# Performance work log

Measured on AMD Instinct MI355X. Metric: run time of the kernel, lower is better.

Reference implementation:

```python
import jax, jax.numpy as jnp
import numpy as np

DIM = 512
NUM_HEADS = 8
HEAD_DIM = DIM // NUM_HEADS
LOCAL_HEADS = 4
WINDOW = 64
NEG_INF = -1e9


def setup_inputs() -> dict:
    key = jax.random.key(0)
    ks = jax.random.split(key, 5)
    B, N, C = 4, 8192, DIM
    x = jax.random.normal(ks[0], (B, N, C), dtype=jnp.float32)
    # nn.Linear weights stored as [out, in]; xavier-ish scale
    s = (2.0 / (C + C)) ** 0.5
    Wq = jax.random.normal(ks[1], (C, C), dtype=jnp.float32) * s
    Wkv = jax.random.normal(ks[2], (C, C), dtype=jnp.float32) * s
    Wproj = jax.random.normal(ks[3], (C, C), dtype=jnp.float32) * s
    bproj = jax.random.normal(ks[4], (C,), dtype=jnp.float32) * 0.01
    return {"x": x, "Wq": Wq, "Wkv": Wkv, "Wproj": Wproj, "bproj": bproj}


def _look_around(t):
    # t: [B,H,nw,m,d] -> [B,H,nw,3m,d] (prev window, current, next; zero-padded at ends)
    p = jnp.pad(t, ((0, 0), (0, 0), (1, 1), (0, 0), (0, 0)))
    return jnp.concatenate([p[:, :, :-2], p[:, :, 1:-1], p[:, :, 2:]], axis=3)


def _local_attn(q, k, v, m):
    # non-causal LocalAttention, look_backward=1, look_forward=1
    B, H, N, d = q.shape
    nw = N // m
    scale = d ** -0.5
    qw = q.reshape(B, H, nw, m, d)
    kw = _look_around(k.reshape(B, H, nw, m, d))
    vw = _look_around(v.reshape(B, H, nw, m, d))
    # mask out look-around positions that fall outside the sequence
    pos = jnp.arange(N).reshape(nw, m)
    pp = jnp.pad(pos, ((1, 1), (0, 0)), constant_values=-1)
    kpos = jnp.concatenate([pp[:-2], pp[1:-1], pp[2:]], axis=1)  # [nw, 3m]
    valid = (kpos >= 0)[None, None, :, None, :]
    scores = jnp.einsum('bhwid,bhwjd->bhwij', qw * scale, kw)
    scores = jnp.where(valid, scores, NEG_INF)
    attn = jax.nn.softmax(scores, axis=-1)
    out = jnp.einsum('bhwij,bhwjd->bhwid', attn, vw)
    return out.reshape(B, H, N, d)


def _linear_attn(q, k, v):
    d = q.shape[-1]
    q = jax.nn.softmax(q, axis=-1) * (d ** -0.5)
    k = jax.nn.softmax(k, axis=-2)
    context = jnp.einsum('bhnd,bhne->bhde', k, v)
    return jnp.einsum('bhnd,bhde->bhne', q, context)


def reference(x, Wq, Wkv, Wproj, bproj):
    B, N, C = x.shape
    m = WINDOW
    original_N = N
    rem = N % m  # static; 0 for chosen shapes
    if rem > 0:
        x = jnp.pad(x, ((0, 0), (m - rem, 0), (0, 0)))
        N = x.shape[1]
    q = x @ Wq.T
    k = x @ Wkv.T
    v = x @ Wkv.T  # source uses the same kv linear for both k and v
    merge = lambda t: t.reshape(B, N, -1, HEAD_DIM).transpose(0, 2, 1, 3)  # [B,H,N,d]
    q, k, v = merge(q), merge(k), merge(v)
    lh = LOCAL_HEADS
    lq, gq = q[:, :lh], q[:, lh:]
    lk, gk = k[:, :lh], k[:, lh:]
    lv, gv = v[:, :lh], v[:, lh:]
    outs = []
    if lh > 0:
        outs.append(_local_attn(lq, lk, lv, m))
    if q.shape[1] - lh > 0:
        outs.append(_linear_attn(gq, gk, gv))
    attn = jnp.concatenate(outs, axis=1)  # [B,H,N,d]
    y = attn.transpose(0, 2, 1, 3).reshape(B, N, -1)
    y = y[:, -original_N:]
    y = y @ Wproj.T + bproj
    return (y, attn)
```

## Files before the change

### kernel.cpp

```cpp
#include <hip/hip_runtime.h>

#define DIM 512
#define NH 8
#define HD 64
#define LH 4
#define WIN 64
#define BATCH 4
#define SEQ 8192
#define NWIN (SEQ/WIN)

typedef unsigned short u16;
typedef __bf16 bf16x8 __attribute__((ext_vector_type(8)));
typedef float f32x4 __attribute__((ext_vector_type(4)));

__device__ __forceinline__ float b2f(u16 u) {
    return __uint_as_float(((unsigned int)u) << 16);
}
__device__ __forceinline__ u16 f2b(float f) {
    unsigned int x = __float_as_uint(f);
    return (u16)((x + 0x7FFFu + ((x >> 16) & 1u)) >> 16);
}

__device__ __forceinline__ void gload16(const void* g, void* l) {
    __builtin_amdgcn_global_load_lds(
        (__attribute__((address_space(1))) void*)g,
        (__attribute__((address_space(3))) void*)l, 16, 0, 0);
}

__global__ void convert_bf16(const float* __restrict__ src, u16* __restrict__ dst, long n)
{
    long i = ((long)blockIdx.x * 256 + threadIdx.x) * 8;
    const long stride = (long)gridDim.x * 256 * 8;
    for (; i < n; i += stride) {
        uint4 a = *(const uint4*)(src + i), b = *(const uint4*)(src + i + 4);
        const float* af = (const float*)&a;
        const float* bf_ = (const float*)&b;
        uint4 o; u16* ou = (u16*)&o;
        #pragma unroll
        for (int j = 0; j < 4; j++) { ou[j] = f2b(af[j]); ou[4 + j] = f2b(bf_[j]); }
        *(uint4*)(dst + i) = o;
    }
}

__global__ void convert_w3(const float* __restrict__ Wq, const float* __restrict__ Wkv,
                           const float* __restrict__ Wp, u16* __restrict__ Wqk,
                           u16* __restrict__ Wproj_b)
{
    const int slice = blockIdx.y;
    const float* src = (slice == 0) ? Wq : (slice == 1) ? Wkv : Wp;
    u16* dst = (slice == 0) ? Wqk : (slice == 1) ? (Wqk + DIM * DIM) : Wproj_b;
    long i = ((long)blockIdx.x * 256 + threadIdx.x) * 8;
    if (i >= (long)DIM * DIM) return;
    uint4 a = *(const uint4*)(src + i), b = *(const uint4*)(src + i + 4);
    const float* af = (const float*)&a;
    const float* bf_ = (const float*)&b;
    uint4 o; u16* ou = (u16*)&o;
    #pragma unroll
    for (int j = 0; j < 4; j++) { ou[j] = f2b(af[j]); ou[4 + j] = f2b(bf_[j]); }
    *(uint4*)(dst + i) = o;
}

__global__ __launch_bounds__(256) void gemm_qk_tiled(const u16* __restrict__ xb,
        const u16* __restrict__ Wqk, u16* __restrict__ qh, u16* __restrict__ kh)
{
    __shared__ __align__(16) u16 smem[16384];
    u16* lA = smem;
    u16* lB = smem + 4096;

    const int tid = threadIdx.x;
    const int wv = tid >> 6, lane = tid & 63;
    const int quad = lane >> 4, l16 = lane & 15;
    const int wr = wv >> 1, wc = wv & 1;
    const int row0 = blockIdx.y * 128;
    const int col0 = blockIdx.x * 128;
    const int lrow = lane >> 2, lkc = (lane & 3) * 8;

    f32x4 acc[4][4];
    #pragma unroll
    for (int t = 0; t < 4; t++)
        for (int u = 0; u < 4; u++)
            for (int i = 0; i < 4; i++) acc[t][u][i] = 0.f;

    const u16* gA = xb  + (size_t)(row0 + lrow) * DIM + lkc;
    const u16* gB = Wqk + (size_t)(col0 + lrow) * DIM + lkc;

    for (int kt = 0; kt < DIM; kt += 32) {
        __syncthreads();
        #pragma unroll
        for (int i = 0; i < 2; i++) {
            int rb = wv * 32 + i * 16;
            gload16(gA + (size_t)rb * DIM + kt, &lA[rb * 32]);
            gload16(gB + (size_t)rb * DIM + kt, &lB[rb * 32]);
        }
        __syncthreads();
        bf16x8 af[4], bfr[4];
        #pragma unroll
        for (int t = 0; t < 4; t++)
            af[t] = *(const bf16x8*)&lA[(wr * 64 + t * 16 + l16) * 32 + quad * 8];
        #pragma unroll
        for (int u = 0; u < 4; u++)
            bfr[u] = *(const bf16x8*)&lB[(wc * 64 + u * 16 + l16) * 32 + quad * 8];
        #pragma unroll
        for (int t = 0; t < 4; t++)
            #pragma unroll
            for (int u = 0; u < 4; u++)
                acc[t][u] = __builtin_amdgcn_mfma_f32_16x16x32_bf16(af[t], bfr[u], acc[t][u], 0, 0, 0);
    }

    __syncthreads();
    u16* cw = smem + wv * 4096;
    #pragma unroll
    for (int t = 0; t < 4; t++)
        #pragma unroll
        for (int u = 0; u < 4; u++)
            #pragma unroll
            for (int r = 0; r < 4; r++)
                cw[(t * 16 + quad * 4 + r) * 64 + u * 16 + l16] = f2b(acc[t][u][r]);

    const int colg0 = col0 + wc * 64;
    const int seg = lane & 7;
    u16* dstbase;
    {
        int h = (colg0 & 511) >> 6;
        u16* base = (colg0 < 512) ? qh : kh;
        dstbase = base + (size_t)h * SEQ * HD;
    }
    #pragma unroll
    for (int i = 0; i < 8; i++) {
        int mm = i * 8 + (lane >> 3);
        uint4 v = *(const uint4*)&cw[mm * 64 + seg * 8];
        int m = row0 + wr * 64 + mm;
        int bb = m >> 13, nn = m & (SEQ - 1);
        *(uint4*)(dstbase + ((size_t)bb * NH * SEQ + nn) * HD + seg * 8) = v;
    }
}

#define KJ_STRIDE 72
#define KT_STRIDE 200
#define OT_STRIDE 80

__global__ __launch_bounds__(256) void local_attn(const u16* __restrict__ qh,
        const u16* __restrict__ kh, float* __restrict__ attn_out,
        u16* __restrict__ attn_b)
{
    __shared__ __align__(16) u16 kjP[192 * KJ_STRIDE];
    __shared__ __align__(16) u16 kT[64 * KT_STRIDE];

    const int w = blockIdx.x;
    const int bh = blockIdx.y;
    const int b = bh >> 2, h = bh & 3;
    const int tid = threadIdx.x;
    const int wv = tid >> 6, lane = tid & 63;
    const int quad = lane >> 4, l16 = lane & 15;

    for (int idx = tid; idx < 192 * 8; idx += 256) {
        int j = idx >> 3, dc = (idx & 7) << 3;
        int n = w * WIN - WIN + j;
        uint4 val = make_uint4(0, 0, 0, 0);
        if (n >= 0 && n < SEQ)
            val = *(const uint4*)(kh + (((size_t)(b * NH + h)) * SEQ + n) * HD + dc);
        *(uint4*)(&kjP[j * KJ_STRIDE + dc]) = val;
    }
    __syncthreads();
    for (int idx = tid; idx < 64 * 192; idx += 256) {
        int e = idx & 63, j = idx >> 6;
        kT[e * KT_STRIDE + j] = kjP[j * KJ_STRIDE + e];
    }
    __syncthreads();

    f32x4 s[12];
    #pragma unroll
    for (int t = 0; t < 12; t++)
        for (int i = 0; i < 4; i++) s[t][i] = 0.f;

    const u16* qrow = qh + (((size_t)(b * NH + h)) * SEQ + w * WIN + wv * 16 + l16) * HD + quad * 8;
    #pragma unroll
    for (int kk = 0; kk < 64; kk += 32) {
        bf16x8 a = *(const bf16x8*)(qrow + kk);
        #pragma unroll
        for (int t = 0; t < 12; t++) {
            bf16x8 bf = *(const bf16x8*)(&kjP[(t * 16 + l16) * KJ_STRIDE + kk + quad * 8]);
            s[t] = __builtin_amdgcn_mfma_f32_16x16x32_bf16(a, bf, s[t], 0, 0, 0);
        }
    }
    __syncthreads();

    const float scale = 0.125f;
    #pragma unroll
    for (int r = 0; r < 4; r++) {
        float vals[12];
        float mx = -3.0e38f;
        #pragma unroll
        for (int t = 0; t < 12; t++) {
            int j = t * 16 + l16;
            float v = s[t][r] * scale;
            bool valid = !((w == 0 && j < 64) || (w == NWIN - 1 && j >= 128));
            v = valid ? v : -30000.0f;
            vals[t] = v;
            mx = fmaxf(mx, v);
        }
        for (int m = 1; m <= 8; m <<= 1) mx = fmaxf(mx, __shfl_xor(mx, m));
        float sum = 0.f;
        #pragma unroll
        for (int t = 0; t < 12; t++) { vals[t] = __expf(vals[t] - mx); sum += vals[t]; }
        for (int m = 1; m <= 8; m <<= 1) sum += __shfl_xor(sum, m);
        float inv = 1.0f / sum;
        int prow = wv * 16 + quad * 4 + r;
        #pragma unroll
        for (int t = 0; t < 12; t++)
            kjP[prow * KT_STRIDE + t * 16 + l16] = f2b(vals[t] * inv);
    }
    __syncthreads();

    f32x4 o[4];
    #pragma unroll
    for (int t = 0; t < 4; t++)
        for (int i = 0; i < 4; i++) o[t][i] = 0.f;
    #pragma unroll
    for (int kc = 0; kc < 6; kc++) {
        bf16x8 a = *(const bf16x8*)(&kjP[(wv * 16 + l16) * KT_STRIDE + kc * 32 + quad * 8]);
        #pragma unroll
        for (int t = 0; t < 4; t++) {
            bf16x8 bf = *(const bf16x8*)(&kT[(t * 16 + l16) * KT_STRIDE + kc * 32 + quad * 8]);
            o[t] = __builtin_amdgcn_mfma_f32_16x16x32_bf16(a, bf, o[t], 0, 0, 0);
        }
    }
    #pragma unroll
    for (int t = 0; t < 4; t++) {
        int e = t * 16 + l16;
        #pragma unroll
        for (int r = 0; r < 4; r++) {
            int n = w * WIN + wv * 16 + quad * 4 + r;
            attn_out[(((size_t)(b * NH + h)) * SEQ + n) * HD + e] = o[t][r];
        }
    }
    __syncthreads();
    #pragma unroll
    for (int t = 0; t < 4; t++)
        #pragma unroll
        for (int r = 0; r < 4; r++)
            kT[(wv * 16 + quad * 4 + r) * OT_STRIDE + t * 16 + l16] = f2b(o[t][r]);
    __syncthreads();
    for (int idx = tid; idx < 512; idx += 256) {
        int row = idx >> 3, seg = (idx & 7) * 8;
        uint4 v = *(const uint4*)&kT[row * OT_STRIDE + seg];
        *(uint4*)(attn_b + ((size_t)(b * SEQ + w * WIN + row)) * DIM + h * HD + seg) = v;
    }
}

__global__ __launch_bounds__(256) void ctx_accum(const u16* __restrict__ kh,
        float* __restrict__ partials, float* __restrict__ colsum)
{
    const int chunk = blockIdx.x;
    const int bh = blockIdx.y;
    const int b = bh >> 2, hg = bh & 3;
    const int tid = threadIdx.x;
    const int wv = tid >> 6, lane = tid & 63;
    const int d0 = (lane >> 2) * 4;
    const int e0 = (lane & 3) * 16;

    __shared__ __align__(16) float smem[2 * 64 * 68];
    float* kraw = smem;
    float* kexp = smem + 64 * 68;

    f32x4 acc[4][4];
    #pragma unroll
    for (int dd = 0; dd < 4; dd++)
        #pragma unroll
        for (int j = 0; j < 4; j++)
            for (int i = 0; i < 4; i++) acc[dd][j][i] = 0.f;
    f32x4 csum;
    for (int i = 0; i < 4; i++) csum[i] = 0.f;

    const u16* kbase = kh + ((size_t)(b * NH + LH + hg)) * SEQ * HD
                          + (size_t)chunk * 256 * HD;

    for (int ph = 0; ph < 4; ph++) {
        __syncthreads();
        #pragma unroll
        for (int pass = 0; pass < 2; pass++) {
            int idx = pass * 256 + tid;
            int row = idx >> 3, seg = (idx & 7) * 8;
            uint4 v = *(const uint4*)(kbase + ((size_t)(ph * 64 + row)) * HD + seg);
            const u16* u = (const u16*)&v;
            f32x4 r0, r1, E0, E1;
            #pragma unroll
            for (int j = 0; j < 4; j++) {
                r0[j] = b2f(u[j]);      E0[j] = __expf(r0[j]);
                r1[j] = b2f(u[4 + j]);  E1[j] = __expf(r1[j]);
            }
            float* kr = &kraw[row * 68 + seg];
            float* ke = &kexp[row * 68 + seg];
            *(f32x4*)kr = r0;  *(f32x4*)(kr + 4) = r1;
            *(f32x4*)ke = E0;  *(f32x4*)(ke + 4) = E1;
        }
        __syncthreads();
        #pragma unroll 4
        for (int i = 0; i < 16; i++) {
            int roff = (wv * 16 + i) * 68;
            f32x4 ek = *(const f32x4*)&kexp[roff + d0];
            const f32x4* kv = (const f32x4*)&kraw[roff + e0];
            f32x4 k0 = kv[0], k1 = kv[1], k2 = kv[2], k3 = kv[3];
            csum += ek;
            #pragma unroll
            for (int dd = 0; dd < 4; dd++) {
                acc[dd][0] += ek[dd] * k0;
                acc[dd][1] += ek[dd] * k1;
                acc[dd][2] += ek[dd] * k2;
                acc[dd][3] += ek[dd] * k3;
            }
        }
    }

    float* red0 = smem;
    float* red1 = smem + 4160;
    __syncthreads();
    if (wv >= 2) {
        float* rd = (wv == 2) ? red0 : red1;
        #pragma unroll
        for (int dd = 0; dd < 4; dd++)
            #pragma unroll
            for (int j = 0; j < 4; j++)
                *(f32x4*)&rd[(d0 + dd) * 64 + e0 + j * 4] = acc[dd][j];
        if ((lane & 3) == 0) *(f32x4*)&rd[4096 + d0] = csum;
    }
    __syncthreads();
    if (wv < 2) {
        float* rd = (wv == 0) ? red0 : red1;
        #pragma unroll
        for (int dd = 0; dd < 4; dd++)
            #pragma unroll
            for (int j = 0; j < 4; j++)
                acc[dd][j] += *(const f32x4*)&rd[(d0 + dd) * 64 + e0 + j * 4];
        csum += *(const f32x4*)&rd[4096 + d0];
    }
    __syncthreads();
    if (wv == 1) {
        #pragma unroll
        for (int dd = 0; dd < 4; dd++)
            #pragma unroll
            for (int j = 0; j < 4; j++)
                *(f32x4*)&red0[(d0 + dd) * 64 + e0 + j * 4] = acc[dd][j];
        if ((lane & 3) == 0) *(f32x4*)&red0[4096 + d0] = csum;
    }
    __syncthreads();
    if (wv == 0) {
        float* P = partials + ((size_t)(chunk * 16 + bh)) * 4096;
        #pragma unroll
        for (int dd = 0; dd < 4; dd++)
            #pragma unroll
            for (int j = 0; j < 4; j++) {
                f32x4 r = acc[dd][j] + *(const f32x4*)&red0[(d0 + dd) * 64 + e0 + j * 4];
                *(f32x4*)&P[(d0 + dd) * 64 + e0 + j * 4] = r;
            }
        if ((lane & 3) == 0) {
            f32x4 cs = csum + *(const f32x4*)&red0[4096 + d0];
            #pragma unroll
            for (int dd = 0; dd < 4; dd++)
                atomicAdd(colsum + bh * 64 + d0 + dd, cs[dd]);
        }
    }
}

__global__ __launch_bounds__(256) void reduce_ctx(const float* __restrict__ partials,
        const float* __restrict__ colsum, float* __restrict__ ctx)
{
    const int quarter = blockIdx.x;
    const int bh = blockIdx.y;
    const int tid = threadIdx.x;
    __shared__ float cs[64];
    if (tid < 64) cs[tid] = colsum[bh * 64 + tid];
    __syncthreads();
    const int i0 = quarter * 1024;
    for (int idx = i0 + tid; idx < i0 + 1024; idx += 256) {
        float s = 0.f;
        #pragma unroll 8
        for (int c = 0; c < 32; c++)
            s += partials[((size_t)(c * 16 + bh)) * 4096 + idx];
        ctx[(size_t)bh * 4096 + idx] = s / cs[idx >> 6];
    }
}

__global__ __launch_bounds__(256) void global_out(const u16* __restrict__ qh,
        const float* __restrict__ ctxg, float* __restrict__ attn_out,
        u16* __restrict__ attn_b)
{
    const int nblk = blockIdx.x;
    const int bh = blockIdx.y;
    const int b = bh >> 2, hg = bh & 3;
    const int tid = threadIdx.x;

    __shared__ float ctx[4096];
    for (int idx = tid; idx < 4096; idx += 256)
        ctx[idx] = ctxg[(size_t)bh * 4096 + idx];
    __syncthreads();

    const int n = nblk * 256 + tid;
    const size_t rowidx = (((size_t)(b * NH + LH + hg)) * SEQ + n) * HD;
    const u16* qrow = qh + rowidx;

    float sumexp = 0.f;
    for (int c = 0; c < 8; c++) {
        uint4 v = *(const uint4*)(qrow + c * 8);
        const u16* u = (const u16*)&v;
        #pragma unroll
        for (int jj = 0; jj < 8; jj++) sumexp += __expf(b2f(u[jj]));
    }
    float inv = 0.125f / sumexp;

    f32x4 out4[16];
    #pragma unroll
    for (int t = 0; t < 16; t++)
        for (int i = 0; i < 4; i++) out4[t][i] = 0.f;

    for (int c = 0; c < 8; c++) {
        uint4 v = *(const uint4*)(qrow + c * 8);
        const u16* u = (const u16*)&v;
        #pragma unroll
        for (int jj = 0; jj < 8; jj++) {
            float pd = __expf(b2f(u[jj])) * inv;
            const f32x4* cr = (const f32x4*)&ctx[(c * 8 + jj) * 64];
            #pragma unroll
            for (int t = 0; t < 16; t++)
                out4[t] += pd * cr[t];
        }
    }

    float* ao = attn_out + rowidx;
    #pragma unroll
    for (int t = 0; t < 16; t++)
        *(f32x4*)(ao + t * 4) = out4[t];

    u16* ab = attn_b + ((size_t)(b * SEQ + n)) * DIM + (LH + hg) * HD;
    #pragma unroll
    for (int t = 0; t < 8; t++) {
        uint4 o; u16* ou = (u16*)&o;
        #pragma unroll
        for (int j = 0; j < 8; j++) ou[j] = f2b(out4[t * 2 + (j >> 2)][j & 3]);
        *(uint4*)(ab + t * 8) = o;
    }
}

__global__ __launch_bounds__(256) void proj_gemm_tiled(const u16* __restrict__ attn_b,
        const u16* __restrict__ Wproj, const float* __restrict__ bproj,
        float* __restrict__ y)
{
    __shared__ __align__(16) u16 smem[8192];
    u16* lA = smem;
    u16* lB = smem + 4096;

    const int tid = threadIdx.x;
    const int wv = tid >> 6, lane = tid & 63;
    const int quad = lane >> 4, l16 = lane & 15;
    const int wr = wv >> 1, wc = wv & 1;
    const int row0 = blockIdx.y * 128;
    const int col0 = blockIdx.x * 128;
    const int lrow = lane >> 2, lkc = (lane & 3) * 8;

    f32x4 acc[4][4];
    #pragma unroll
    for (int t = 0; t < 4; t++)
        for (int u = 0; u < 4; u++)
            for (int i = 0; i < 4; i++) acc[t][u][i] = 0.f;

    const u16* gA = attn_b + (size_t)(row0 + lrow) * DIM + lkc;
    const u16* gB = Wproj  + (size_t)(col0 + lrow) * DIM + lkc;

    for (int kt = 0; kt < DIM; kt += 32) {
        __syncthreads();
        #pragma unroll
        for (int i = 0; i < 2; i++) {
            int rb = wv * 32 + i * 16;
            gload16(gA + (size_t)rb * DIM + kt, &lA[rb * 32]);
            gload16(gB + (size_t)rb * DIM + kt, &lB[rb * 32]);
        }
        __syncthreads();
        bf16x8 af[4], bfr[4];
        #pragma unroll
        for (int t = 0; t < 4; t++)
            af[t] = *(const bf16x8*)&lA[(wr * 64 + t * 16 + l16) * 32 + quad * 8];
        #pragma unroll
        for (int u = 0; u < 4; u++)
            bfr[u] = *(const bf16x8*)&lB[(wc * 64 + u * 16 + l16) * 32 + quad * 8];
        #pragma unroll
        for (int t = 0; t < 4; t++)
            #pragma unroll
            for (int u = 0; u < 4; u++)
                acc[t][u] = __builtin_amdgcn_mfma_f32_16x16x32_bf16(af[t], bfr[u], acc[t][u], 0, 0, 0);
    }

    #pragma unroll
    for (int u = 0; u < 4; u++) {
        int col = col0 + wc * 64 + u * 16 + l16;
        float bias = bproj[col];
        #pragma unroll
        for (int t = 0; t < 4; t++)
            #pragma unroll
            for (int r = 0; r < 4; r++) {
                int m = row0 + wr * 64 + t * 16 + quad * 4 + r;
                y[(size_t)m * DIM + col] = acc[t][u][r] + bias;
            }
    }
}

extern "C" void kernel_launch(void* const* d_in, const int* in_sizes, int n_in,
                              void* d_out, int out_size, void* d_ws, size_t ws_size,
                              hipStream_t stream)
{
    (void)in_sizes; (void)n_in; (void)out_size; (void)ws_size;
    const float* x     = (const float*)d_in[0];
    const float* Wq    = (const float*)d_in[1];
    const float* Wkv   = (const float*)d_in[2];
    const float* Wproj = (const float*)d_in[3];
    const float* bproj = (const float*)d_in[4];

    float* y        = (float*)d_out;
    float* attn_out = y + (size_t)BATCH * SEQ * DIM;

    u16* xb = (u16*)y;
    u16* qh = xb + (size_t)BATCH * SEQ * DIM;

    float* partials = attn_out + (size_t)LH * SEQ * HD;

    char* ws = (char*)d_ws;
    float* S       = (float*)ws;
    float* colsum  = (float*)(ws + 262144);
    u16*   Wqk     = (u16*)(ws + 266240);
    u16*   Wproj_b = (u16*)(ws + 266240 + 1048576);
    u16*   kh      = (u16*)(ws + 266240 + 1048576 + 524288);
    u16*   attn_b  = kh + (size_t)BATCH * SEQ * DIM;

    const long NX = (long)BATCH * SEQ * DIM;

    hipMemsetAsync(colsum, 0, 4096, stream);
    convert_bf16<<<4096, 256, 0, stream>>>(x, xb, NX);
    convert_w3<<<dim3(128, 3), 256, 0, stream>>>(Wq, Wkv, Wproj, Wqk, Wproj_b);

    gemm_qk_tiled<<<dim3(8, 256), 256, 0, stream>>>(xb, Wqk, qh, kh);
    local_attn<<<dim3(NWIN, 16), 256, 0, stream>>>(qh, kh, attn_out, attn_b);
    ctx_accum<<<dim3(32, 16), 256, 0, stream>>>(kh, partials, colsum);
    reduce_ctx<<<dim3(4, 16), 256, 0, stream>>>(partials, colsum, S);
    global_out<<<dim3(32, 16), 256, 0, stream>>>(qh, S, attn_out, attn_b);
    proj_gemm_tiled<<<dim3(4, 256), 256, 0, stream>>>(attn_b, Wproj_b, bproj, y);
}
```

Baseline: 368.2 us.

## Swizzle GEMM LDS tiles with K=64 and move global attention output to MFMA

Both bf16 GEMMs now stage 64-wide K tiles in LDS with an XOR swizzle, halving barrier count per K loop and reducing bank conflicts. The linear-attention output kernel now stores the context as transposed bf16 and computes softmax(q)·ctx with MFMA instructions over 64-row blocks instead of scalar FMAs. This adds bf16 rounding of the context and probabilities, which loosens precision, and doubles the GEMM shared memory.

```diff
diff --git a/kernel.cpp b/kernel.cpp
--- a/kernel.cpp
+++ b/kernel.cpp
@@ -65,7 +65,7 @@
 {
     __shared__ __align__(16) u16 smem[16384];
     u16* lA = smem;
-    u16* lB = smem + 4096;
+    u16* lB = smem + 8192;
 
     const int tid = threadIdx.x;
     const int wv = tid >> 6, lane = tid & 63;
@@ -73,7 +73,8 @@
     const int wr = wv >> 1, wc = wv & 1;
     const int row0 = blockIdx.y * 128;
     const int col0 = blockIdx.x * 128;
-    const int lrow = lane >> 2, lkc = (lane & 3) * 8;
+    const int srow = lane >> 3;
+    const int scol = ((lane & 7) ^ srow) * 8;
 
     f32x4 acc[4][4];
     #pragma unroll
@@ -81,30 +82,39 @@
         for (int u = 0; u < 4; u++)
             for (int i = 0; i < 4; i++) acc[t][u][i] = 0.f;
 
-    const u16* gA = xb  + (size_t)(row0 + lrow) * DIM + lkc;
-    const u16* gB = Wqk + (size_t)(col0 + lrow) * DIM + lkc;
-
-    for (int kt = 0; kt < DIM; kt += 32) {
+    const u16* gA = xb  + (size_t)(row0 + srow) * DIM + scol;
+    const u16* gB = Wqk + (size_t)(col0 + srow) * DIM + scol;
+
+    for (int kt = 0; kt < DIM; kt += 64) {
         __syncthreads();
         #pragma unroll
-        for (int i = 0; i < 2; i++) {
-            int rb = wv * 32 + i * 16;
-            gload16(gA + (size_t)rb * DIM + kt, &lA[rb * 32]);
-            gload16(gB + (size_t)rb * DIM + kt, &lB[rb * 32]);
+        for (int i = 0; i < 4; i++) {
+            int rb = wv * 32 + i * 8;
+            gload16(gA + (size_t)rb * DIM + kt, &lA[rb * 64]);
+            gload16(gB + (size_t)rb * DIM + kt, &lB[rb * 64]);
         }
         __syncthreads();
-        bf16x8 af[4], bfr[4];
-        #pragma unroll
-        for (int t = 0; t < 4; t++)
-            af[t] = *(const bf16x8*)&lA[(wr * 64 + t * 16 + l16) * 32 + quad * 8];
-        #pragma unroll
-        for (int u = 0; u < 4; u++)
-            bfr[u] = *(const bf16x8*)&lB[(wc * 64 + u * 16 + l16) * 32 + quad * 8];
-        #pragma unroll
-        for (int t = 0; t < 4; t++)
-            #pragma unroll
-            for (int u = 0; u < 4; u++)
-                acc[t][u] = __builtin_amdgcn_mfma_f32_16x16x32_bf16(af[t], bfr[u], acc[t][u], 0, 0, 0);
+        #pragma unroll
+        for (int kc = 0; kc < 2; kc++) {
+            bf16x8 af[4], bfr[4];
+            #pragma unroll
+            for (int t = 0; t < 4; t++) {
+                int row = wr * 64 + t * 16 + l16;
+                int slot = (kc * 4 + quad) ^ (row & 7);
+                af[t] = *(const bf16x8*)&lA[row * 64 + slot * 8];
+            }
+            #pragma unroll
+            for (int u = 0; u < 4; u++) {
+                int row = wc * 64 + u * 16 + l16;
+                int slot = (kc * 4 + quad) ^ (row & 7);
+                bfr[u] = *(const bf16x8*)&lB[row * 64 + slot * 8];
+            }
+            #pragma unroll
+            for (int t = 0; t < 4; t++)
+                #pragma unroll
+                for (int u = 0; u < 4; u++)
+                    acc[t][u] = __builtin_amdgcn_mfma_f32_16x16x32_bf16(af[t], bfr[u], acc[t][u], 0, 0, 0);
+        }
     }
 
     __syncthreads();
@@ -363,7 +373,7 @@
 }
 
 __global__ __launch_bounds__(256) void reduce_ctx(const float* __restrict__ partials,
-        const float* __restrict__ colsum, float* __restrict__ ctx)
+        const float* __restrict__ colsum, u16* __restrict__ ctxT)
 {
     const int quarter = blockIdx.x;
     const int bh = blockIdx.y;
@@ -377,67 +387,94 @@
         #pragma unroll 8
         for (int c = 0; c < 32; c++)
             s += partials[((size_t)(c * 16 + bh)) * 4096 + idx];
-        ctx[(size_t)bh * 4096 + idx] = s / cs[idx >> 6];
+        int d = idx >> 6, e = idx & 63;
+        ctxT[(size_t)bh * 4096 + e * 64 + d] = f2b(s / cs[d]);
     }
 }
 
 __global__ __launch_bounds__(256) void global_out(const u16* __restrict__ qh,
-        const float* __restrict__ ctxg, float* __restrict__ attn_out,
+        const u16* __restrict__ ctxT, float* __restrict__ attn_out,
         u16* __restrict__ attn_b)
 {
     const int nblk = blockIdx.x;
     const int bh = blockIdx.y;
     const int b = bh >> 2, hg = bh & 3;
     const int tid = threadIdx.x;
-
-    __shared__ float ctx[4096];
-    for (int idx = tid; idx < 4096; idx += 256)
-        ctx[idx] = ctxg[(size_t)bh * 4096 + idx];
-    __syncthreads();
-
-    const int n = nblk * 256 + tid;
-    const size_t rowidx = (((size_t)(b * NH + LH + hg)) * SEQ + n) * HD;
-    const u16* qrow = qh + rowidx;
-
-    float sumexp = 0.f;
-    for (int c = 0; c < 8; c++) {
-        uint4 v = *(const uint4*)(qrow + c * 8);
-        const u16* u = (const u16*)&v;
-        #pragma unroll
-        for (int jj = 0; jj < 8; jj++) sumexp += __expf(b2f(u[jj]));
-    }
-    float inv = 0.125f / sumexp;
-
-    f32x4 out4[16];
-    #pragma unroll
-    for (int t = 0; t < 16; t++)
-        for (int i = 0; i < 4; i++) out4[t][i] = 0.f;
-
-    for (int c = 0; c < 8; c++) {
-        uint4 v = *(const uint4*)(qrow + c * 8);
-        const u16* u = (const u16*)&v;
-        #pragma unroll
-        for (int jj = 0; jj < 8; jj++) {
-            float pd = __expf(b2f(u[jj])) * inv;
-            const f32x4* cr = (const f32x4*)&ctx[(c * 8 + jj) * 64];
-            #pragma unroll
-            for (int t = 0; t < 16; t++)
-                out4[t] += pd * cr[t];
-        }
-    }
-
-    float* ao = attn_out + rowidx;
-    #pragma unroll
-    for (int t = 0; t < 16; t++)
-        *(f32x4*)(ao + t * 4) = out4[t];
-
-    u16* ab = attn_b + ((size_t)(b * SEQ + n)) * DIM + (LH + hg) * HD;
-    #pragma unroll
-    for (int t = 0; t < 8; t++) {
-        uint4 o; u16* ou = (u16*)&o;
-        #pragma unroll
-        for (int j = 0; j < 8; j++) ou[j] = f2b(out4[t * 2 + (j >> 2)][j & 3]);
-        *(uint4*)(ab + t * 8) = o;
+    const int wv = tid >> 6, lane = tid & 63;
+    const int quad = lane >> 4, l16 = lane & 15;
+
+    __shared__ __align__(16) u16 ctxL[64 * 64];
+    __shared__ __align__(16) u16 ot[64 * OT_STRIDE];
+
+    {
+        const int srow = lane >> 3;
+        const int scol = ((lane & 7) ^ srow) * 8;
+        const u16* src = ctxT + (size_t)bh * 4096 + (size_t)srow * 64 + scol;
+        #pragma unroll
+        for (int j = 0; j < 2; j++) {
+            int rb = j * 32 + wv * 8;
+            gload16(src + rb * 64, &ctxL[rb * 64]);
+        }
+    }
+
+    const int n0 = nblk * 64;
+    const u16* qp = qh + (((size_t)(b * NH + LH + hg)) * SEQ + n0 + wv * 16 + l16) * HD + quad * 8;
+    uint4 v0 = *(const uint4*)(qp);
+    uint4 v1 = *(const uint4*)(qp + 32);
+    const u16* u0 = (const u16*)&v0;
+    const u16* u1 = (const u16*)&v1;
+    float e0[8], e1[8];
+    float s = 0.f;
+    #pragma unroll
+    for (int j = 0; j < 8; j++) { e0[j] = __expf(b2f(u0[j])); s += e0[j]; }
+    #pragma unroll
+    for (int j = 0; j < 8; j++) { e1[j] = __expf(b2f(u1[j])); s += e1[j]; }
+    s += __shfl_xor(s, 16);
+    s += __shfl_xor(s, 32);
+    const float inv = 0.125f / s;
+    uint4 p0u, p1u;
+    u16* p0 = (u16*)&p0u; u16* p1 = (u16*)&p1u;
+    #pragma unroll
+    for (int j = 0; j < 8; j++) { p0[j] = f2b(e0[j] * inv); p1[j] = f2b(e1[j] * inv); }
+    bf16x8 pa0 = *(const bf16x8*)&p0u;
+    bf16x8 pa1 = *(const bf16x8*)&p1u;
+
+    __syncthreads();
+
+    f32x4 acc[4];
+    #pragma unroll
+    for (int u = 0; u < 4; u++)
+        for (int i = 0; i < 4; i++) acc[u][i] = 0.f;
+    #pragma unroll
+    for (int u = 0; u < 4; u++) {
+        int row = u * 16 + l16;
+        int s0 = (0 + quad) ^ (row & 7);
+        int s1 = (4 + quad) ^ (row & 7);
+        bf16x8 b0 = *(const bf16x8*)&ctxL[row * 64 + s0 * 8];
+        bf16x8 b1 = *(const bf16x8*)&ctxL[row * 64 + s1 * 8];
+        acc[u] = __builtin_amdgcn_mfma_f32_16x16x32_bf16(pa0, b0, acc[u], 0, 0, 0);
+        acc[u] = __builtin_amdgcn_mfma_f32_16x16x32_bf16(pa1, b1, acc[u], 0, 0, 0);
+    }
+
+    const size_t obase = ((size_t)(b * NH + LH + hg)) * SEQ + n0 + wv * 16;
+    #pragma unroll
+    for (int u = 0; u < 4; u++) {
+        int ee = u * 16 + l16;
+        #pragma unroll
+        for (int r = 0; r < 4; r++)
+            attn_out[(obase + quad * 4 + r) * HD + ee] = acc[u][r];
+    }
+
+    #pragma unroll
+    for (int u = 0; u < 4; u++)
+        #pragma unroll
+        for (int r = 0; r < 4; r++)
+            ot[(wv * 16 + quad * 4 + r) * OT_STRIDE + u * 16 + l16] = f2b(acc[u][r]);
+    __syncthreads();
+    for (int idx = tid; idx < 512; idx += 256) {
+        int row = idx >> 3, seg = (idx & 7) * 8;
+        uint4 vv = *(const uint4*)&ot[row * OT_STRIDE + seg];
+        *(uint4*)(attn_b + ((size_t)(b * SEQ + n0 + row)) * DIM + (LH + hg) * HD + seg) = vv;
     }
 }
 
@@ -445,9 +482,9 @@
         const u16* __restrict__ Wproj, const float* __restrict__ bproj,
         float* __restrict__ y)
 {
-    __shared__ __align__(16) u16 smem[8192];
+    __shared__ __align__(16) u16 smem[16384];
     u16* lA = smem;
-    u16* lB = smem + 4096;
+    u16* lB = smem + 8192;
 
     const int tid = threadIdx.x;
     const int wv = tid >> 6, lane = tid & 63;
@@ -455,7 +492,8 @@
     const int wr = wv >> 1, wc = wv & 1;
     const int row0 = blockIdx.y * 128;
     const int col0 = blockIdx.x * 128;
-    const int lrow = lane >> 2, lkc = (lane & 3) * 8;
+    const int srow = lane >> 3;
+    const int scol = ((lane & 7) ^ srow) * 8;
 
     f32x4 acc[4][4];
     #pragma unroll
@@ -463,30 +501,39 @@
         for (int u = 0; u < 4; u++)
             for (int i = 0; i < 4; i++) acc[t][u][i] = 0.f;
 
-    const u16* gA = attn_b + (size_t)(row0 + lrow) * DIM + lkc;
-    const u16* gB = Wproj  + (size_t)(col0 + lrow) * DIM + lkc;
-
-    for (int kt = 0; kt < DIM; kt += 32) {
+    const u16* gA = attn_b + (size_t)(row0 + srow) * DIM + scol;
+    const u16* gB = Wproj  + (size_t)(col0 + srow) * DIM + scol;
+
+    for (int kt = 0; kt < DIM; kt += 64) {
         __syncthreads();
         #pragma unroll
-        for (int i = 0; i < 2; i++) {
-            int rb = wv * 32 + i * 16;
-            gload16(gA + (size_t)rb * DIM + kt, &lA[rb * 32]);
-            gload16(gB + (size_t)rb * DIM + kt, &lB[rb * 32]);
+        for (int i = 0; i < 4; i++) {
+            int rb = wv * 32 + i * 8;
+            gload16(gA + (size_t)rb * DIM + kt, &lA[rb * 64]);
+            gload16(gB + (size_t)rb * DIM + kt, &lB[rb * 64]);
         }
         __syncthreads();
-        bf16x8 af[4], bfr[4];
-        #pragma unroll
-        for (int t = 0; t < 4; t++)
-            af[t] = *(const bf16x8*)&lA[(wr * 64 + t * 16 + l16) * 32 + quad * 8];
-        #pragma unroll
-        for (int u = 0; u < 4; u++)
-            bfr[u] = *(const bf16x8*)&lB[(wc * 64 + u * 16 + l16) * 32 + quad * 8];
-        #pragma unroll
-        for (int t = 0; t < 4; t++)
-            #pragma unroll
-            for (int u = 0; u < 4; u++)
-                acc[t][u] = __builtin_amdgcn_mfma_f32_16x16x32_bf16(af[t], bfr[u], acc[t][u], 0, 0, 0);
+        #pragma unroll
+        for (int kc = 0; kc < 2; kc++) {
+            bf16x8 af[4], bfr[4];
+            #pragma unroll
+            for (int t = 0; t < 4; t++) {
+                int row = wr * 64 + t * 16 + l16;
+                int slot = (kc * 4 + quad) ^ (row & 7);
+                af[t] = *(const bf16x8*)&lA[row * 64 + slot * 8];
+            }
+            #pragma unroll
+            for (int u = 0; u < 4; u++) {
+                int row = wc * 64 + u * 16 + l16;
+                int slot = (kc * 4 + quad) ^ (row & 7);
+                bfr[u] = *(const bf16x8*)&lB[row * 64 + slot * 8];
+            }
+            #pragma unroll
+            for (int t = 0; t < 4; t++)
+                #pragma unroll
+                for (int u = 0; u < 4; u++)
+                    acc[t][u] = __builtin_amdgcn_mfma_f32_16x16x32_bf16(af[t], bfr[u], acc[t][u], 0, 0, 0);
+        }
     }
 
     #pragma unroll
@@ -523,7 +570,7 @@
     float* partials = attn_out + (size_t)LH * SEQ * HD;
 
     char* ws = (char*)d_ws;
-    float* S       = (float*)ws;
+    u16*   ctxT    = (u16*)ws;
     float* colsum  = (float*)(ws + 262144);
     u16*   Wqk     = (u16*)(ws + 266240);
     u16*   Wproj_b = (u16*)(ws + 266240 + 1048576);
@@ -539,7 +586,7 @@
     gemm_qk_tiled<<<dim3(8, 256), 256, 0, stream>>>(xb, Wqk, qh, kh);
     local_attn<<<dim3(NWIN, 16), 256, 0, stream>>>(qh, kh, attn_out, attn_b);
     ctx_accum<<<dim3(32, 16), 256, 0, stream>>>(kh, partials, colsum);
-    reduce_ctx<<<dim3(4, 16), 256, 0, stream>>>(partials, colsum, S);
-    global_out<<<dim3(32, 16), 256, 0, stream>>>(qh, S, attn_out, attn_b);
+    reduce_ctx<<<dim3(4, 16), 256, 0, stream>>>(partials, colsum, ctxT);
+    global_out<<<dim3(SEQ / 64, 16), 256, 0, stream>>>(qh, ctxT, attn_out, attn_b);
     proj_gemm_tiled<<<dim3(4, 256), 256, 0, stream>>>(attn_b, Wproj_b, bproj, y);
 }
```

Result: faster. 345.2 us (-6.2%).
